# Kernel tuning notes

Measured on AMD Instinct MI355X. Metric: run time of the kernel, lower is better.

## Reference

```python
import jax, jax.numpy as jnp
import numpy as np

B, D, H, C, T = 65536, 512, 256, 100, 10
EPS = 0.01  # halt_epsilon


def setup_inputs() -> dict:
    key = jax.random.key(0)
    ks = jax.random.split(key, 10)
    sD = 1.0 / np.sqrt(D)
    sH = 1.0 / np.sqrt(H)
    return {
        "x": jax.random.normal(ks[0], (B, D), dtype=jnp.float32),
        # GRUCell params (PyTorch layout: rows chunked as [r; z; n])
        "W_ih": jax.random.uniform(ks[1], (3 * H, D), minval=-sD, maxval=sD, dtype=jnp.float32),
        "W_hh": jax.random.uniform(ks[2], (3 * H, H), minval=-sH, maxval=sH, dtype=jnp.float32),
        "b_ih": jax.random.uniform(ks[3], (3 * H,), minval=-sH, maxval=sH, dtype=jnp.float32),
        "b_hh": jax.random.uniform(ks[4], (3 * H,), minval=-sH, maxval=sH, dtype=jnp.float32),
        # halting unit
        "W_halt": jax.random.uniform(ks[5], (1, H), minval=-sH, maxval=sH, dtype=jnp.float32),
        "b_halt": jax.random.uniform(ks[6], (1,), minval=-sH, maxval=sH, dtype=jnp.float32),
        # readout
        "W_ro": jax.random.uniform(ks[7], (C, H), minval=-sH, maxval=sH, dtype=jnp.float32),
        "b_ro": jax.random.uniform(ks[8], (C,), minval=-sH, maxval=sH, dtype=jnp.float32),
    }


def _act_forward(x, W_ih, W_hh, b_ih, b_hh, W_halt, b_halt, W_ro, b_ro):
    dt = x.dtype
    thresh = jnp.asarray(1.0 - EPS, dt)
    # x is static across ponder steps -> precompute input projection once
    x_proj = x @ W_ih.T + b_ih                       # [B, 3H]
    xr, xz, xn = jnp.split(x_proj, 3, axis=-1)

    def step(carry, _):
        h, cum, rem, nup, acc = carry
        h_proj = h @ W_hh.T + b_hh                   # [B, 3H]
        hr, hz, hn = jnp.split(h_proj, 3, axis=-1)
        r = jax.nn.sigmoid(xr + hr)
        z = jax.nn.sigmoid(xz + hz)
        n = jnp.tanh(xn + r * hn)
        h_new = (1.0 - z) * n + z * h                # GRUCell update
        halt = jax.nn.sigmoid(h_new @ W_halt.T + b_halt)[:, 0]  # [B]
        logits_t = h_new @ W_ro.T + b_ro             # [B, C]
        still = (cum < thresh).astype(dt)
        new_halt = halt * still
        would = (cum + new_halt > thresh).astype(dt)
        remainder = (1.0 - cum) * would * still
        step_w = new_halt * (1.0 - would) + remainder
        cum2 = cum + step_w
        acc2 = acc + step_w[:, None] * h_new
        return (h_new, cum2, rem + remainder, nup + still, acc2), (h_new, halt, logits_t)

    zB = jnp.zeros((x.shape[0],), dt)
    init = (jnp.zeros((x.shape[0], W_hh.shape[1]), dt), zB, zB, zB,
            jnp.zeros((x.shape[0], W_hh.shape[1]), dt))
    (h, cum, remainders, n_updates, acc), (h_seq, halt_seq, logits_seq) = jax.lax.scan(
        step, init, None, length=T)
    logits = acc @ W_ro.T + b_ro                     # [B, C]
    ponder_cost = n_updates.mean() + remainders.mean()
    # scan stacks on axis 0 (time) -> move to dim 1 as torch.stack(dim=1)
    h_seq = jnp.swapaxes(h_seq, 0, 1)                # [B, T, H]
    halt_seq = jnp.swapaxes(halt_seq, 0, 1)          # [B, T]
    logits_seq = jnp.swapaxes(logits_seq, 0, 1)      # [B, T, C]
    return logits, ponder_cost, n_updates, h_seq, halt_seq, logits_seq


def reference(x, W_ih, W_hh, b_ih, b_hh, W_halt, b_halt, W_ro, b_ro):
    return _act_forward(x, W_ih, W_hh, b_ih, b_hh, W_halt, b_halt, W_ro, b_ro)
```

## Files before the change

kernel.cpp:

```cpp
#include <hip/hip_runtime.h>
#include <cmath>


namespace {
constexpr int B = 65536, D = 512, H = 256, C = 100, T = 10;

constexpr long OUT_LOGITS = 0;
constexpr long OUT_PONDER = (long)B * C;
constexpr long OUT_NUP    = OUT_PONDER + 1;
constexpr long OUT_HSEQ   = OUT_NUP + B;
constexpr long OUT_HALT   = OUT_HSEQ + (long)B * T * H;
constexpr long OUT_LSEQ   = OUT_HALT + (long)B * T;

constexpr long NIH  = 768L * D;
constexpr long NHH  = 768L * H;
constexpr long NAUG = 112L * H;

constexpr long WS_XP   = 0;
constexpr long WS_W16  = WS_XP + (long)B * 768;
constexpr long W_HALV  = 2 * (NIH + NHH + NAUG);
constexpr long WS_HL   = WS_W16 + (W_HALV + 1) / 2;
constexpr long WS_HP4  = WS_HL + (long)B * T;
constexpr long WS_NUPB = WS_HP4 + 4L * B * T;
constexpr long WS_REMB = WS_NUPB + B;
constexpr long WS_H16  = WS_REMB + B;
constexpr long H16_PER_T = 1024L * 32768;

constexpr float SC  = 256.f;
constexpr float ISC = 1.f / 256.f;
constexpr float SB  = 1.f / 65536.f;
}

typedef __attribute__((ext_vector_type(8))) _Float16 h8;
typedef __attribute__((ext_vector_type(4))) _Float16 h4;
typedef __attribute__((ext_vector_type(4))) float f4;

#define MFMA16(A, Bo, Cc) __builtin_amdgcn_mfma_f32_16x16x32_f16(A, Bo, Cc, 0, 0, 0)
#define PROD3(a, Ah, Al, Bh, Bl)                                               \
  a = MFMA16(Al, Bh, a);                                                       \
  a = MFMA16(Ah, Bl, a);                                                       \
  a = MFMA16(Ah, Bh, a);

__device__ __forceinline__ float sigmoidf_(float x) {
  if (x >= 0.f) { return 1.f / (1.f + expf(-x)); }
  float e = expf(x);
  return e / (1.f + e);
}

__device__ __forceinline__ void gload_lds16(const _Float16* g, _Float16* l) {
  __builtin_amdgcn_global_load_lds(
      (const __attribute__((address_space(1))) unsigned int*)g,
      (__attribute__((address_space(3))) unsigned int*)l, 16, 0, 0);
}

__global__ void k_prep(const float* __restrict__ wih_s, const float* __restrict__ whh_s,
                       const float* __restrict__ wro, const float* __restrict__ whalt,
                       _Float16* __restrict__ wr) {
  long idx = (long)blockIdx.x * 256 + threadIdx.x;
  if (idx < NIH) {
    float xs = wih_s[idx] * SC;
    _Float16 h = (_Float16)xs;
    _Float16 l = (_Float16)(xs - (float)h);
    wr[idx] = h; wr[NIH + idx] = l;
  }
  if (idx < NHH) {
    float xs = whh_s[idx] * SC;
    _Float16 h = (_Float16)xs;
    _Float16 l = (_Float16)(xs - (float)h);
    long b = 2 * NIH;
    wr[b + idx] = h; wr[b + NHH + idx] = l;
  }
  if (idx < NAUG) {
    int row = (int)(idx >> 8), k = (int)(idx & 255);
    float x = (row < C) ? wro[row * 256 + k] : ((row == C) ? whalt[k] : 0.f);
    float xs = x * SC;
    _Float16 h = (_Float16)xs;
    _Float16 l = (_Float16)(xs - (float)h);
    long b = 2 * (NIH + NHH);
    wr[b + idx] = h; wr[b + NAUG + idx] = l;
  }
}

__device__ __forceinline__ void stageA16(const float* __restrict__ src,
                                         _Float16* As0, _Float16* As1,
                                         int o) {
#pragma unroll
  for (int i = 0; i < 4; ++i) {
    float4 v = ((const float4*)src)[i];
    float vv[4] = {v.x, v.y, v.z, v.w};
    h4 hh, ll;
#pragma unroll
    for (int c = 0; c < 4; ++c) {
      float sv = vv[c] * SC;
      _Float16 h = (_Float16)sv;
      hh[c] = h;
      ll[c] = (_Float16)(sv - (float)h);
    }
    *(h4*)&As0[o + i * 4] = hh;
    *(h4*)&As1[o + i * 4] = ll;
  }
}

__global__ __launch_bounds__(256, 3) void k_xproj(
    const float* __restrict__ x, const _Float16* __restrict__ wih,
    const float* __restrict__ b_ih, float* __restrict__ xpt) {
  __shared__ __align__(16) _Float16 As0[128 * 40], As1[128 * 40];
  __shared__ __align__(16) _Float16 Bs[2][192 * 32];
  const int tid = threadIdx.x;
  const int w = tid >> 6, l = tid & 63;
  const int lr = l & 15, lq = l >> 4;
  const int bid = blockIdx.x;
  const int gid = (bid & 7) * 256 + (bid >> 3);
  const int c0 = (gid & 3) * 64;
  const int rb = (gid >> 2) * 128;

  f4 acc[8][3];
#pragma unroll
  for (int i = 0; i < 8; ++i)
#pragma unroll
    for (int g = 0; g < 3; ++g) acc[i][g] = (f4)0.f;

  for (int kc = 0; kc < 16; ++kc) {
    const int k0 = kc * 32;
    __syncthreads();
    {
      const int row = tid >> 1, kk0 = (tid & 1) * 16;
      stageA16(x + (long)(rb + row) * D + k0 + kk0, As0, As1, row * 40 + kk0);
    }
#pragma unroll
    for (int j = 0; j < 6; ++j) {
      int chunk = w * 6 + j;
      int plane = chunk / 12;
      int rem = chunk - plane * 12;
      int scol = rem * 16 + (l >> 2);
      int kq = l & 3;
      int gcol = (scol >> 6) * 256 + c0 + (scol & 63);
      gload_lds16(wih + (long)plane * NIH + (long)gcol * D + k0 + kq * 8,
                  &Bs[plane][rem * 512]);
    }
    __syncthreads();
    h8 Bh[3], Bl[3];
#pragma unroll
    for (int g = 0; g < 3; ++g) {
      Bh[g] = *(const h8*)&Bs[0][(g * 64 + w * 16 + lr) * 32 + lq * 8];
      Bl[g] = *(const h8*)&Bs[1][(g * 64 + w * 16 + lr) * 32 + lq * 8];
    }
#pragma unroll
    for (int i = 0; i < 8; ++i) {
      h8 Ah = *(const h8*)&As0[(i * 16 + lr) * 40 + lq * 8];
      h8 Al = *(const h8*)&As1[(i * 16 + lr) * 40 + lq * 8];
#pragma unroll
      for (int g = 0; g < 3; ++g) { PROD3(acc[i][g], Ah, Al, Bh[g], Bl[g]); }
    }
  }
  const int ch = c0 + w * 16 + lr;
  const int strip = gid & 3;
  float bi[3] = {b_ih[ch], b_ih[256 + ch], b_ih[512 + ch]};
  const long xoff = (long)(lq * 256 + w * 64 + lr * 4);
#pragma unroll
  for (int i = 0; i < 8; ++i) {
    const long t4s = (long)((gid >> 2) * 2 + (i >> 2)) * 4 + strip;
#pragma unroll
    for (int g = 0; g < 3; ++g) {
      float4 v = make_float4(fmaf(acc[i][g][0], SB, bi[g]),
                             fmaf(acc[i][g][1], SB, bi[g]),
                             fmaf(acc[i][g][2], SB, bi[g]),
                             fmaf(acc[i][g][3], SB, bi[g]));
      *(float4*)&xpt[((t4s * 3 + g) * 4 + (i & 3)) * 1024 + xoff] = v;
    }
  }
}

__global__ __launch_bounds__(256, 4) void k_gru(
    const _Float16* __restrict__ whh, const float* __restrict__ xpt,
    const float* __restrict__ b_hh, const float* __restrict__ w_halt,
    float* __restrict__ out, _Float16* __restrict__ h16,
    float* __restrict__ hp4, int t) {
  __shared__ __align__(16) _Float16 As[2][64 * 32];
  __shared__ __align__(16) _Float16 Bs[2][192 * 32];
  __shared__ float lds_hp[64][4];
  const int tid = threadIdx.x;
  const int w = tid >> 6, l = tid & 63;
  const int lr = l & 15, lq = l >> 4;
  const int bid = blockIdx.x;
  const int gid = (bid & 7) * 512 + (bid >> 3);
  const int strip = gid & 3;
  const int c0 = strip * 64;
  const int rb = (gid >> 2) * 64;
  const long tilebase = (long)(rb >> 6) * 32768;
  const int ch = c0 + w * 16 + lr;
  const int kc_h = ch >> 5;

  f4 acc[4][3];
  float ho[4][4];
  float xnv[4][4];
  const long t4s = (long)(gid >> 2) * 4 + strip;
  const long xoff = (long)(lq * 256 + w * 64 + lr * 4);
#pragma unroll
  for (int i = 0; i < 4; ++i) {
    float4 vr = *(const float4*)&xpt[((t4s * 3 + 0) * 4 + i) * 1024 + xoff];
    float4 vz = *(const float4*)&xpt[((t4s * 3 + 1) * 4 + i) * 1024 + xoff];
    float4 vn = *(const float4*)&xpt[((t4s * 3 + 2) * 4 + i) * 1024 + xoff];
    acc[i][0][0] = vr.x * 65536.f; acc[i][0][1] = vr.y * 65536.f;
    acc[i][0][2] = vr.z * 65536.f; acc[i][0][3] = vr.w * 65536.f;
    acc[i][1][0] = vz.x * 65536.f; acc[i][1][1] = vz.y * 65536.f;
    acc[i][1][2] = vz.z * 65536.f; acc[i][1][3] = vz.w * 65536.f;
    xnv[i][0] = vn.x; xnv[i][1] = vn.y; xnv[i][2] = vn.z; xnv[i][3] = vn.w;
    acc[i][2] = (f4)0.f;
#pragma unroll
    for (int reg = 0; reg < 4; ++reg) ho[i][reg] = 0.f;
  }

  if (t > 0) {
    const _Float16* h16r = h16 + (long)(t - 1) * H16_PER_T + tilebase;
    for (int kc = 0; kc < 8; ++kc) {
      const int k0 = kc * 32;
      __syncthreads();
#pragma unroll
      for (int j = 0; j < 2; ++j) {
        int c = w * 2 + j;
        int plane = c >> 2;
        int cc = c & 3;
        gload_lds16(h16r + (long)kc * 4096 + plane * 2048 + cc * 512 + l * 8,
                    &As[plane][cc * 512]);
      }
#pragma unroll
      for (int j = 0; j < 6; ++j) {
        int chunk = w * 6 + j;
        int plane = chunk / 12;
        int rem = chunk - plane * 12;
        int scol = rem * 16 + (l >> 2);
        int kq = l & 3;
        int gcol = (scol >> 6) * 256 + c0 + (scol & 63);
        gload_lds16(whh + (long)plane * NHH + (long)gcol * H + k0 + kq * 8,
                    &Bs[plane][rem * 512]);
      }
      __syncthreads();
      h8 Bh[3], Bl[3];
#pragma unroll
      for (int g = 0; g < 3; ++g) {
        Bh[g] = *(const h8*)&Bs[0][(g * 64 + w * 16 + lr) * 32 + lq * 8];
        Bl[g] = *(const h8*)&Bs[1][(g * 64 + w * 16 + lr) * 32 + lq * 8];
      }
#pragma unroll
      for (int i = 0; i < 4; ++i) {
        h8 Ah = *(const h8*)&As[0][(i * 16 + lr) * 32 + lq * 8];
        h8 Al = *(const h8*)&As[1][(i * 16 + lr) * 32 + lq * 8];
#pragma unroll
        for (int g = 0; g < 3; ++g) { PROD3(acc[i][g], Ah, Al, Bh[g], Bl[g]); }
      }
      if (kc == kc_h) {
#pragma unroll
        for (int i = 0; i < 4; ++i)
#pragma unroll
          for (int reg = 0; reg < 4; ++reg) {
            int rloc = i * 16 + lq * 4 + reg;
            ho[i][reg] = ((float)As[0][rloc * 32 + (ch & 31)] +
                          (float)As[1][rloc * 32 + (ch & 31)]) * ISC;
          }
      }
    }
  }

  const float bhr = b_hh[ch], bhz = b_hh[256 + ch], bhn = b_hh[512 + ch];
  const float whv = w_halt[ch];
  const long h16base = (long)t * H16_PER_T + tilebase + (long)kc_h * 4096 + (ch & 31);
#pragma unroll
  for (int i = 0; i < 4; ++i)
#pragma unroll
    for (int reg = 0; reg < 4; ++reg) {
      const int rloc = i * 16 + lq * 4 + reg;
      const long row = rb + rloc;
      float rr = sigmoidf_(fmaf(acc[i][0][reg], SB, bhr));
      float zz = sigmoidf_(fmaf(acc[i][1][reg], SB, bhz));
      float nn = tanhf(xnv[i][reg] + rr * fmaf(acc[i][2][reg], SB, bhn));
      float hv = (1.f - zz) * nn + zz * ho[i][reg];
      out[OUT_HSEQ + row * (T * H) + (long)t * H + ch] = hv;
      float sv = hv * SC;
      _Float16 hi = (_Float16)sv;
      _Float16 lo = (_Float16)(sv - (float)hi);
      h16[h16base + (long)rloc * 32] = hi;
      h16[h16base + 2048 + (long)rloc * 32] = lo;
      float p = hv * whv;
#pragma unroll
      for (int m = 1; m < 16; m <<= 1) p += __shfl_xor(p, m, 64);
      if (lr == 0) lds_hp[rloc][w] = p;
    }
  __syncthreads();
  if (tid < 64)
    hp4[((long)t * 4 + strip) * B + rb + tid] =
        ((lds_hp[tid][0] + lds_hp[tid][1]) + (lds_hp[tid][2] + lds_hp[tid][3]));
}

__global__ __launch_bounds__(256, 4) void k_lseq(
    const _Float16* __restrict__ h16, const _Float16* __restrict__ waug,
    const float* __restrict__ b_ro, float* __restrict__ lseq) {
  __shared__ __align__(16) _Float16 As[128 * 32];
  __shared__ __align__(16) _Float16 Bs[112 * 32];
  const int tid = threadIdx.x;
  const int w = tid >> 6, l = tid & 63;
  const int lr = l & 15, lq = l >> 4;
  const int t = blockIdx.x >> 9;
  const int btile = blockIdx.x & 511;
  const _Float16* h16r = h16 + (long)t * H16_PER_T + (long)btile * 65536;

  f4 acc[2][7];
#pragma unroll
  for (int i = 0; i < 2; ++i)
#pragma unroll
    for (int j = 0; j < 7; ++j) acc[i][j] = (f4)0.f;

  for (int kc = 0; kc < 8; ++kc) {
    const int k0 = kc * 32;
    __syncthreads();
#pragma unroll
    for (int j = 0; j < 2; ++j) {
      int c = w * 2 + j;
      gload_lds16(h16r + (long)(c >> 2) * 32768 + (long)kc * 4096 + (c & 3) * 512 + l * 8,
                  &As[c * 512]);
    }
#pragma unroll
    for (int j = 0; j < 2; ++j) {
      int chunk = w + j * 4;
      if (chunk < 7) {
        int scol = chunk * 16 + (l >> 2);
        int kq = l & 3;
        gload_lds16(waug + (long)scol * H + k0 + kq * 8, &Bs[chunk * 512]);
      }
    }
    __syncthreads();
    h8 Af[2];
#pragma unroll
    for (int i = 0; i < 2; ++i)
      Af[i] = *(const h8*)&As[(w * 32 + i * 16 + lr) * 32 + lq * 8];
#pragma unroll
    for (int j = 0; j < 7; ++j) {
      h8 Bf = *(const h8*)&Bs[(j * 16 + lr) * 32 + lq * 8];
#pragma unroll
      for (int i = 0; i < 2; ++i) acc[i][j] = MFMA16(Af[i], Bf, acc[i][j]);
    }
  }
#pragma unroll
  for (int j = 0; j < 7; ++j) {
    const int col = j * 16 + lr;
    if (col < C) {
      const float br = b_ro[col];
#pragma unroll
      for (int i = 0; i < 2; ++i)
#pragma unroll
        for (int reg = 0; reg < 4; ++reg) {
          long b = (long)btile * 128 + w * 32 + i * 16 + lq * 4 + reg;
          lseq[(b * T + t) * C + col] = fmaf(acc[i][j][reg], SB, br);
        }
    }
  }
}

__global__ void k_act(const float* __restrict__ hp4, const float* __restrict__ b_halt,
                      float* __restrict__ out, float* __restrict__ swb,
                      float* __restrict__ nupb, float* __restrict__ remb) {
  const long b = (long)blockIdx.x * 256 + threadIdx.x;
  const float bh = b_halt[0];
  float cum = 0.f, rem = 0.f, nu = 0.f;
#pragma unroll
  for (int t = 0; t < T; ++t) {
    float v = bh + hp4[((long)t * 4 + 0) * B + b] + hp4[((long)t * 4 + 1) * B + b] +
              hp4[((long)t * 4 + 2) * B + b] + hp4[((long)t * 4 + 3) * B + b];
    float halt = sigmoidf_(v);
    out[OUT_HALT + b * T + t] = halt;
    float still = (cum < 0.99f) ? 1.f : 0.f;
    float nh = halt * still;
    float would = ((cum + nh) > 0.99f) ? 1.f : 0.f;
    float rema = (1.f - cum) * would * still;
    float swv = nh * (1.f - would) + rema;
    cum += swv; rem += rema; nu += still;
    swb[b * T + t] = swv;
  }
  nupb[b] = nu; remb[b] = rem;
}

__global__ void k_logits(const float* __restrict__ lseq, const float* __restrict__ swb,
                         const float* __restrict__ b_ro, const float* __restrict__ nupb,
                         float* __restrict__ out) {
  const long b = blockIdx.x;
  const int tid = threadIdx.x;
  if (tid < C) {
    float br = b_ro[tid];
    float s = br;
#pragma unroll
    for (int t = 0; t < T; ++t) {
      float sw = swb[b * T + t];
      s = fmaf(sw, lseq[(b * T + t) * C + tid] - br, s);
    }
    out[OUT_LOGITS + b * C + tid] = s;
  } else if (tid == C) {
    out[OUT_NUP + b] = nupb[b];
  }
}

__global__ void k_ponder(const float* __restrict__ nupb, const float* __restrict__ remb,
                         float* __restrict__ out) {
  __shared__ float sm[4];
  float s = 0.f;
  for (int i = threadIdx.x; i < B; i += 256) s += nupb[i] + remb[i];
#pragma unroll
  for (int m = 1; m < 64; m <<= 1) s += __shfl_xor(s, m, 64);
  int w = threadIdx.x >> 6;
  if ((threadIdx.x & 63) == 0) sm[w] = s;
  __syncthreads();
  if (threadIdx.x == 0)
    out[OUT_PONDER] = (sm[0] + sm[1] + sm[2] + sm[3]) * (1.f / (float)B);
}

extern "C" void kernel_launch(void* const* d_in, const int* in_sizes, int n_in,
                              void* d_out, int out_size, void* d_ws, size_t ws_size,
                              hipStream_t stream) {
  const float* x      = (const float*)d_in[0];
  const float* W_ih   = (const float*)d_in[1];
  const float* W_hh   = (const float*)d_in[2];
  const float* b_ih   = (const float*)d_in[3];
  const float* b_hh   = (const float*)d_in[4];
  const float* W_halt = (const float*)d_in[5];
  const float* b_halt = (const float*)d_in[6];
  const float* W_ro   = (const float*)d_in[7];
  const float* b_ro   = (const float*)d_in[8];
  float* out = (float*)d_out;
  float* ws  = (float*)d_ws;

  float* xpt       = ws + WS_XP;
  _Float16* w16    = (_Float16*)(ws + WS_W16);
  _Float16* wih16  = w16;
  _Float16* whh16  = w16 + 2 * NIH;
  _Float16* waug16 = w16 + 2 * (NIH + NHH);
  float* swb  = ws + WS_HL;
  float* hp4  = ws + WS_HP4;
  float* nupb = ws + WS_NUPB;
  float* remb = ws + WS_REMB;
  _Float16* h16 = (_Float16*)(ws + WS_H16);

  k_prep<<<(int)((NIH + 255) / 256), 256, 0, stream>>>(W_ih, W_hh, W_ro, W_halt, w16);
  k_xproj<<<2048, 256, 0, stream>>>(x, wih16, b_ih, xpt);
  for (int t = 0; t < T; ++t)
    k_gru<<<4096, 256, 0, stream>>>(whh16, xpt, b_hh, W_halt, out, h16, hp4, t);
  k_lseq<<<512 * T, 256, 0, stream>>>(h16, waug16, b_ro, out + OUT_LSEQ);
  k_act<<<B / 256, 256, 0, stream>>>(hp4, b_halt, out, swb, nupb, remb);
  k_logits<<<B, 128, 0, stream>>>(out + OUT_LSEQ, swb, b_ro, nupb, out);
  k_ponder<<<1, 256, 0, stream>>>(nupb, remb, out);
}
```

Measured before the change: 2.189 ms.

## Double-buffer LDS tiles in GRU recurrent GEMM to overlap loads with MFMA

Gives the per-step GRU kernel two LDS buffers for the h and W_hh tiles. The next K-chunk is prefetched with direct global-to-LDS loads while the current chunk is computed, using raw barriers and explicit vmcnt waits instead of __syncthreads. The goal is to hide global load latency behind the split-fp16 matrix products. LDS use doubles and the occupancy hint drops from 4 to 2 blocks per CU, so fewer waves are resident to hide latency. Correctness also depends on the hand-set vmcnt count matching the 8 loads issued per thread.

```diff
diff --git a/kernel.cpp b/kernel.cpp
--- a/kernel.cpp
+++ b/kernel.cpp
@@ -171,13 +171,13 @@
   }
 }
 
-__global__ __launch_bounds__(256, 4) void k_gru(
+__global__ __launch_bounds__(256, 2) void k_gru(
     const _Float16* __restrict__ whh, const float* __restrict__ xpt,
     const float* __restrict__ b_hh, const float* __restrict__ w_halt,
     float* __restrict__ out, _Float16* __restrict__ h16,
     float* __restrict__ hp4, int t) {
-  __shared__ __align__(16) _Float16 As[2][64 * 32];
-  __shared__ __align__(16) _Float16 Bs[2][192 * 32];
+  __shared__ __align__(16) _Float16 As[2][2][64 * 32];
+  __shared__ __align__(16) _Float16 Bs[2][2][192 * 32];
   __shared__ float lds_hp[64][4];
   const int tid = threadIdx.x;
   const int w = tid >> 6, l = tid & 63;
@@ -213,39 +213,54 @@
 
   if (t > 0) {
     const _Float16* h16r = h16 + (long)(t - 1) * H16_PER_T + tilebase;
+
+#define STAGE_AB(buf, kc_)                                                      \
+    {                                                                           \
+      const int k0_ = (kc_) * 32;                                               \
+      _Pragma("unroll")                                                         \
+      for (int j = 0; j < 2; ++j) {                                             \
+        int c = w * 2 + j;                                                      \
+        int plane = c >> 2;                                                     \
+        int cc = c & 3;                                                         \
+        gload_lds16(h16r + (long)(kc_) * 4096 + plane * 2048 + cc * 512 + l * 8,\
+                    &As[buf][plane][cc * 512]);                                 \
+      }                                                                         \
+      _Pragma("unroll")                                                         \
+      for (int j = 0; j < 6; ++j) {                                             \
+        int chunk = w * 6 + j;                                                  \
+        int plane = chunk / 12;                                                 \
+        int rem = chunk - plane * 12;                                           \
+        int scol = rem * 16 + (l >> 2);                                         \
+        int kq = l & 3;                                                         \
+        int gcol = (scol >> 6) * 256 + c0 + (scol & 63);                        \
+        gload_lds16(whh + (long)plane * NHH + (long)gcol * H + k0_ + kq * 8,    \
+                    &Bs[buf][plane][rem * 512]);                                \
+      }                                                                         \
+    }
+
+    STAGE_AB(0, 0);
+#pragma unroll
     for (int kc = 0; kc < 8; ++kc) {
-      const int k0 = kc * 32;
-      __syncthreads();
-#pragma unroll
-      for (int j = 0; j < 2; ++j) {
-        int c = w * 2 + j;
-        int plane = c >> 2;
-        int cc = c & 3;
-        gload_lds16(h16r + (long)kc * 4096 + plane * 2048 + cc * 512 + l * 8,
-                    &As[plane][cc * 512]);
+      const int cur = kc & 1;
+      __builtin_amdgcn_s_barrier();
+      if (kc < 7) {
+        STAGE_AB(cur ^ 1, kc + 1);
+        asm volatile("s_waitcnt vmcnt(8)" ::: "memory");
+      } else {
+        asm volatile("s_waitcnt vmcnt(0)" ::: "memory");
       }
-#pragma unroll
-      for (int j = 0; j < 6; ++j) {
-        int chunk = w * 6 + j;
-        int plane = chunk / 12;
-        int rem = chunk - plane * 12;
-        int scol = rem * 16 + (l >> 2);
-        int kq = l & 3;
-        int gcol = (scol >> 6) * 256 + c0 + (scol & 63);
-        gload_lds16(whh + (long)plane * NHH + (long)gcol * H + k0 + kq * 8,
-                    &Bs[plane][rem * 512]);
+      __builtin_amdgcn_s_barrier();
+      __builtin_amdgcn_sched_barrier(0);
+      h8 Bh[3], Bl[3];
+#pragma unroll
+      for (int g = 0; g < 3; ++g) {
+        Bh[g] = *(const h8*)&Bs[cur][0][(g * 64 + w * 16 + lr) * 32 + lq * 8];
+        Bl[g] = *(const h8*)&Bs[cur][1][(g * 64 + w * 16 + lr) * 32 + lq * 8];
       }
-      __syncthreads();
-      h8 Bh[3], Bl[3];
-#pragma unroll
-      for (int g = 0; g < 3; ++g) {
-        Bh[g] = *(const h8*)&Bs[0][(g * 64 + w * 16 + lr) * 32 + lq * 8];
-        Bl[g] = *(const h8*)&Bs[1][(g * 64 + w * 16 + lr) * 32 + lq * 8];
-      }
 #pragma unroll
       for (int i = 0; i < 4; ++i) {
-        h8 Ah = *(const h8*)&As[0][(i * 16 + lr) * 32 + lq * 8];
-        h8 Al = *(const h8*)&As[1][(i * 16 + lr) * 32 + lq * 8];
+        h8 Ah = *(const h8*)&As[cur][0][(i * 16 + lr) * 32 + lq * 8];
+        h8 Al = *(const h8*)&As[cur][1][(i * 16 + lr) * 32 + lq * 8];
 #pragma unroll
         for (int g = 0; g < 3; ++g) { PROD3(acc[i][g], Ah, Al, Bh[g], Bl[g]); }
       }
@@ -255,11 +270,12 @@
 #pragma unroll
           for (int reg = 0; reg < 4; ++reg) {
             int rloc = i * 16 + lq * 4 + reg;
-            ho[i][reg] = ((float)As[0][rloc * 32 + (ch & 31)] +
-                          (float)As[1][rloc * 32 + (ch & 31)]) * ISC;
+            ho[i][reg] = ((float)As[cur][0][rloc * 32 + (ch & 31)] +
+                          (float)As[cur][1][rloc * 32 + (ch & 31)]) * ISC;
           }
       }
     }
+#undef STAGE_AB
   }
 
   const float bhr = b_hh[ch], bhz = b_hh[256 + ch], bhn = b_hh[512 + ch];
```

Measured after the change: 2.383 ms. +8.9%, slower.
